# Performance work log

Measured on AMD Instinct MI355X. Metric: run time of the kernel, lower is better.

Reference implementation:

```python
import jax, jax.numpy as jnp
import numpy as np

VOCAB = 50257
EMBED = 128
N_HOPS = 3
MAX_STORY_LEN = 50


def setup_inputs() -> dict:
    key = jax.random.key(0)
    ks = jax.random.split(key, 10)
    B, n, T_c, T_q = 64, 50, 20, 20
    stories = jax.random.randint(ks[0], (B, n, T_c), 0, VOCAB)
    questions = jax.random.randint(ks[1], (B, T_q), 0, VOCAB)
    stories_masks = jax.random.randint(ks[2], (B, n, T_c), 0, 2)
    # Embedding tables, N(0, 0.1), padding_idx=0 row zeroed (as in torch nn.Embedding padding_idx)
    def emb(k, rows):
        w = 0.1 * jax.random.normal(k, (rows, EMBED), dtype=jnp.float32)
        return w.at[0].set(0.0)
    W_A = emb(ks[3], VOCAB)
    W_B = emb(ks[4], VOCAB)
    W_C = emb(ks[5], VOCAB)
    W_AT = emb(ks[6], MAX_STORY_LEN + 1)
    W_CT = emb(ks[7], MAX_STORY_LEN + 1)
    # nn.Linear(embed, vocab): weight [vocab, embed], bias [vocab]
    lim = 1.0 / np.sqrt(EMBED)
    W_lin = jax.random.uniform(ks[8], (VOCAB, EMBED), minval=-lim, maxval=lim, dtype=jnp.float32)
    b_lin = jax.random.uniform(ks[9], (VOCAB,), minval=-lim, maxval=lim, dtype=jnp.float32)
    return {"stories": stories, "questions": questions, "stories_masks": stories_masks,
            "W_A": W_A, "W_B": W_B, "W_C": W_C, "W_AT": W_AT, "W_CT": W_CT,
            "W_lin": W_lin, "b_lin": b_lin}


def reference(stories, questions, stories_masks, W_A, W_B, W_C, W_AT, W_CT, W_lin, b_lin):
    B, n, T_c = stories.shape
    # temporal index: sentence i -> i+1 if it contains any real token (mask==0), else 0 (padding)
    word_len = (stories_masks == 0).sum(axis=2)                      # [B, n]
    te_idx = jnp.arange(1, n + 1)[None, :] * (word_len >= 1)         # [B, n]
    # question embedding (basic encoding: sum over tokens)
    u = W_B[questions].sum(axis=1)                                   # [B, d]
    # memories/contexts: embeddings are identical every hop, compute once
    m = W_A[stories].sum(axis=2) + W_AT[te_idx]                      # [B, n, d]
    c = W_C[stories].sum(axis=2) + W_CT[te_idx]                      # [B, n, d]
    for _ in range(N_HOPS):
        score = jnp.einsum('bnd,bd->bn', m, u)                       # [B, n]
        probs = jax.nn.softmax(score, axis=1)
        o = jnp.einsum('bnd,bn->bd', c, probs)                       # [B, d]
        u = u + o
    return u @ W_lin.T + b_lin                                       # [B, vocab]
```

## Files before the change

kernel.cpp:

```cpp
#include <hip/hip_runtime.h>
#include <hip/hip_bf16.h>

#define VOCAB 50257
#define EMBED 128
#define NSENT 50
#define TC 20
#define TQ 20
#define BATCH 64
#define NHOPS 3

typedef __bf16 bf16x8 __attribute__((ext_vector_type(8)));
typedef float  f32x4v __attribute__((ext_vector_type(4)));

__global__ void __launch_bounds__(256) k_embed(
    const int* __restrict__ stories, const int* __restrict__ masks,
    const int* __restrict__ questions,
    const float* __restrict__ W_A, const float* __restrict__ W_B,
    const float* __restrict__ W_C,
    const float* __restrict__ W_AT, const float* __restrict__ W_CT,
    float* __restrict__ ws_m, float* __restrict__ ws_c, float* __restrict__ ws_u)
{
    const int blk = blockIdx.x;
    const int tid = threadIdx.x;
    if (blk < BATCH * NSENT) {
        const int b = blk / NSENT;
        const int i = blk % NSENT;
        const int* mrow = masks + (b * NSENT + i) * TC;
        int cnt = 0;
        #pragma unroll
        for (int t = 0; t < TC; t++) cnt += (mrow[t] == 0);
        const int te = (cnt >= 1) ? (i + 1) : 0;

        const int* srow = stories + (b * NSENT + i) * TC;
        const int table = tid >> 7;
        const int d = tid & 127;
        const float* T  = table ? W_C  : W_A;
        const float* TT = table ? W_CT : W_AT;
        float acc = TT[te * EMBED + d];
        #pragma unroll
        for (int t = 0; t < TC; t++) {
            const int tok = srow[t];
            acc += T[tok * EMBED + d];
        }
        float* dst = table ? ws_c : ws_m;
        dst[(b * NSENT + i) * EMBED + d] = acc;
    } else {
        const int b = blk - BATCH * NSENT;
        if (tid < EMBED) {
            const int* qrow = questions + b * TQ;
            float acc = 0.f;
            #pragma unroll
            for (int t = 0; t < TQ; t++) acc += W_B[qrow[t] * EMBED + tid];
            ws_u[b * EMBED + tid] = acc;
        }
    }
}

__global__ void __launch_bounds__(256) k_hops(
    const float* __restrict__ ws_m, const float* __restrict__ ws_c,
    const float* __restrict__ ws_u, __bf16* __restrict__ ws_ubf)
{
    __shared__ float smc[2 * NSENT * EMBED];
    __shared__ float su[EMBED];
    __shared__ float sp[64];
    __shared__ float ssc[64];

    const int b = blockIdx.x;
    const int tid = threadIdx.x;

    const f32x4v* gm = (const f32x4v*)(ws_m + b * NSENT * EMBED);
    const f32x4v* gc = (const f32x4v*)(ws_c + b * NSENT * EMBED);
    f32x4v* s4 = (f32x4v*)smc;
    for (int idx = tid; idx < NSENT * EMBED / 4; idx += 256) {
        s4[idx] = gm[idx];
        s4[NSENT * EMBED / 4 + idx] = gc[idx];
    }
    if (tid < EMBED) su[tid] = ws_u[b * EMBED + tid];
    __syncthreads();

    const int wave = tid >> 6, lane = tid & 63;
    for (int hop = 0; hop < NHOPS; hop++) {
        for (int i = wave; i < NSENT; i += 4) {
            float s = smc[i * EMBED + lane] * su[lane]
                    + smc[i * EMBED + 64 + lane] * su[64 + lane];
            #pragma unroll
            for (int off = 32; off >= 1; off >>= 1) s += __shfl_xor(s, off);
            if (lane == 0) ssc[i] = s;
        }
        __syncthreads();
        if (tid < 64) {
            float v = (tid < NSENT) ? ssc[tid] : -1e30f;
            float mx = v;
            #pragma unroll
            for (int off = 32; off >= 1; off >>= 1) mx = fmaxf(mx, __shfl_xor(mx, off));
            float e = (tid < NSENT) ? expf(v - mx) : 0.f;
            float sum = e;
            #pragma unroll
            for (int off = 32; off >= 1; off >>= 1) sum += __shfl_xor(sum, off);
            sp[tid] = e / sum;
        }
        __syncthreads();
        if (tid < EMBED) {
            float o = 0.f;
            for (int i = 0; i < NSENT; i++)
                o += smc[NSENT * EMBED + i * EMBED + tid] * sp[i];
            su[tid] += o;
        }
        __syncthreads();
    }
    if (tid < EMBED) ws_ubf[b * EMBED + tid] = (__bf16)su[tid];
}

__global__ void __launch_bounds__(256) k_out(
    const __bf16* __restrict__ u_bf, const float* __restrict__ W_lin,
    const float* __restrict__ b_lin, float* __restrict__ out)
{
    const int tid  = threadIdx.x;
    const int wave = tid >> 6, lane = tid & 63;
    const int m    = lane & 15;
    const int quad = lane >> 4;
    const int v0   = blockIdx.x * 64 + wave * 16;
    const int v    = v0 + m;
    const int vc   = (v < VOCAB) ? v : (VOCAB - 1);

    f32x4v acc[4] = { {0.f,0.f,0.f,0.f}, {0.f,0.f,0.f,0.f},
                      {0.f,0.f,0.f,0.f}, {0.f,0.f,0.f,0.f} };

    const float* wrow = W_lin + (long)vc * EMBED;
    #pragma unroll
    for (int kc = 0; kc < 4; kc++) {
        const int k0 = kc * 32 + quad * 8;
        f32x4v w0 = *(const f32x4v*)(wrow + k0);
        f32x4v w1 = *(const f32x4v*)(wrow + k0 + 4);
        bf16x8 wb;
        wb[0] = (__bf16)w0[0]; wb[1] = (__bf16)w0[1];
        wb[2] = (__bf16)w0[2]; wb[3] = (__bf16)w0[3];
        wb[4] = (__bf16)w1[0]; wb[5] = (__bf16)w1[1];
        wb[6] = (__bf16)w1[2]; wb[7] = (__bf16)w1[3];
        #pragma unroll
        for (int bt = 0; bt < 4; bt++) {
            bf16x8 ab = *(const bf16x8*)(u_bf + (bt * 16 + m) * EMBED + k0);
            acc[bt] = __builtin_amdgcn_mfma_f32_16x16x32_bf16(ab, wb, acc[bt], 0, 0, 0);
        }
    }

    const float bl = b_lin[vc];
    if (v < VOCAB) {
        #pragma unroll
        for (int bt = 0; bt < 4; bt++) {
            #pragma unroll
            for (int r = 0; r < 4; r++) {
                const int bb = bt * 16 + quad * 4 + r;
                out[(long)bb * VOCAB + v] = acc[bt][r] + bl;
            }
        }
    }
}

extern "C" void kernel_launch(void* const* d_in, const int* in_sizes, int n_in,
                              void* d_out, int out_size, void* d_ws, size_t ws_size,
                              hipStream_t stream) {
    const int*   stories   = (const int*)d_in[0];
    const int*   questions = (const int*)d_in[1];
    const int*   masks     = (const int*)d_in[2];
    const float* W_A       = (const float*)d_in[3];
    const float* W_B       = (const float*)d_in[4];
    const float* W_C       = (const float*)d_in[5];
    const float* W_AT      = (const float*)d_in[6];
    const float* W_CT      = (const float*)d_in[7];
    const float* W_lin     = (const float*)d_in[8];
    const float* b_lin     = (const float*)d_in[9];
    float* out = (float*)d_out;

    float* ws    = (float*)d_ws;
    float* ws_m  = ws;
    float* ws_c  = ws + BATCH * NSENT * EMBED;
    float* ws_u  = ws + 2 * BATCH * NSENT * EMBED;
    __bf16* ws_ubf = (__bf16*)(ws + 2 * BATCH * NSENT * EMBED + BATCH * EMBED);

    k_embed<<<dim3(BATCH * NSENT + BATCH), dim3(256), 0, stream>>>(
        stories, masks, questions, W_A, W_B, W_C, W_AT, W_CT, ws_m, ws_c, ws_u);
    k_hops<<<dim3(BATCH), dim3(256), 0, stream>>>(ws_m, ws_c, ws_u, ws_ubf);
    k_out<<<dim3((VOCAB + 63) / 64), dim3(256), 0, stream>>>(ws_ubf, W_lin, b_lin, out);
}
```

Measured before the change: 163.2 us.

## Vectorize embedding gathers, split hop reduction, stage output tile through LDS

The embedding kernel now gathers rows with float4 loads, with groups of 32 threads each summing a subset of tokens, and reduces the partial sums through shared memory. In the hop kernel all 256 threads take part in the weighted context sum, split across two halves of the sentences. The output GEMM handles 128 vocab columns per block, stages results in a padded shared tile, and writes coalesced rows with nontemporal stores. These target uncoalesced scalar gathers, idle threads, and the strided scattered output writes, at the cost of extra shared memory and block syncs.

Measured after the change: 161.7 us. No clear change (-0.9%).

```diff
diff --git a/kernel.cpp b/kernel.cpp
--- a/kernel.cpp
+++ b/kernel.cpp
@@ -20,8 +20,12 @@
     const float* __restrict__ W_AT, const float* __restrict__ W_CT,
     float* __restrict__ ws_m, float* __restrict__ ws_c, float* __restrict__ ws_u)
 {
+    __shared__ float sred[8][128];
     const int blk = blockIdx.x;
     const int tid = threadIdx.x;
+    const int grp = tid >> 5;
+    const int gl  = tid & 31;
+
     if (blk < BATCH * NSENT) {
         const int b = blk / NSENT;
         const int i = blk % NSENT;
@@ -32,26 +36,40 @@
         const int te = (cnt >= 1) ? (i + 1) : 0;
 
         const int* srow = stories + (b * NSENT + i) * TC;
-        const int table = tid >> 7;
-        const int d = tid & 127;
-        const float* T  = table ? W_C  : W_A;
-        const float* TT = table ? W_CT : W_AT;
-        float acc = TT[te * EMBED + d];
-        #pragma unroll
-        for (int t = 0; t < TC; t++) {
-            const int tok = srow[t];
-            acc += T[tok * EMBED + d];
-        }
-        float* dst = table ? ws_c : ws_m;
-        dst[(b * NSENT + i) * EMBED + d] = acc;
+        const int table = grp >> 2;
+        const int sub   = grp & 3;
+        const float* T = table ? W_C : W_A;
+
+        f32x4v acc = {0.f, 0.f, 0.f, 0.f};
+        #pragma unroll
+        for (int t = 0; t < 5; t++) {
+            const int tok = srow[sub + t * 4];
+            acc += *(const f32x4v*)(T + (long)tok * EMBED + gl * 4);
+        }
+        *(f32x4v*)&sred[grp][gl * 4] = acc;
+        __syncthreads();
+
+        const int tb = tid >> 7, d = tid & 127;
+        const float* TT = tb ? W_CT : W_AT;
+        float v = sred[tb * 4 + 0][d] + sred[tb * 4 + 1][d]
+                + sred[tb * 4 + 2][d] + sred[tb * 4 + 3][d]
+                + TT[te * EMBED + d];
+        float* dst = tb ? ws_c : ws_m;
+        dst[(b * NSENT + i) * EMBED + d] = v;
     } else {
         const int b = blk - BATCH * NSENT;
+        f32x4v acc = {0.f, 0.f, 0.f, 0.f};
+        for (int t = grp; t < TQ; t += 8) {
+            const int tok = questions[b * TQ + t];
+            acc += *(const f32x4v*)(W_B + (long)tok * EMBED + gl * 4);
+        }
+        *(f32x4v*)&sred[grp][gl * 4] = acc;
+        __syncthreads();
         if (tid < EMBED) {
-            const int* qrow = questions + b * TQ;
-            float acc = 0.f;
-            #pragma unroll
-            for (int t = 0; t < TQ; t++) acc += W_B[qrow[t] * EMBED + tid];
-            ws_u[b * EMBED + tid] = acc;
+            float v = 0.f;
+            #pragma unroll
+            for (int g = 0; g < 8; g++) v += sred[g][tid];
+            ws_u[b * EMBED + tid] = v;
         }
     }
 }
@@ -64,6 +82,7 @@
     __shared__ float su[EMBED];
     __shared__ float sp[64];
     __shared__ float ssc[64];
+    __shared__ float spo[2][EMBED];
 
     const int b = blockIdx.x;
     const int tid = threadIdx.x;
@@ -79,6 +98,7 @@
     __syncthreads();
 
     const int wave = tid >> 6, lane = tid & 63;
+    const int d128 = tid & 127, hf = tid >> 7;
     for (int hop = 0; hop < NHOPS; hop++) {
         for (int i = wave; i < NSENT; i += 4) {
             float s = smc[i * EMBED + lane] * su[lane]
@@ -100,59 +120,79 @@
             sp[tid] = e / sum;
         }
         __syncthreads();
-        if (tid < EMBED) {
+        {
             float o = 0.f;
-            for (int i = 0; i < NSENT; i++)
-                o += smc[NSENT * EMBED + i * EMBED + tid] * sp[i];
-            su[tid] += o;
-        }
+            #pragma unroll
+            for (int k = 0; k < 25; k++) {
+                const int i = hf * 25 + k;
+                o += smc[NSENT * EMBED + i * EMBED + d128] * sp[i];
+            }
+            spo[hf][d128] = o;
+        }
+        __syncthreads();
+        if (tid < EMBED) su[tid] += spo[0][tid] + spo[1][tid];
         __syncthreads();
     }
     if (tid < EMBED) ws_ubf[b * EMBED + tid] = (__bf16)su[tid];
 }
 
+#define VT 128
 __global__ void __launch_bounds__(256) k_out(
     const __bf16* __restrict__ u_bf, const float* __restrict__ W_lin,
     const float* __restrict__ b_lin, float* __restrict__ out)
 {
+    __shared__ float sT[64][VT + 1];
+
     const int tid  = threadIdx.x;
     const int wave = tid >> 6, lane = tid & 63;
     const int m    = lane & 15;
     const int quad = lane >> 4;
-    const int v0   = blockIdx.x * 64 + wave * 16;
-    const int v    = v0 + m;
-    const int vc   = (v < VOCAB) ? v : (VOCAB - 1);
-
-    f32x4v acc[4] = { {0.f,0.f,0.f,0.f}, {0.f,0.f,0.f,0.f},
-                      {0.f,0.f,0.f,0.f}, {0.f,0.f,0.f,0.f} };
-
-    const float* wrow = W_lin + (long)vc * EMBED;
+    const int vbase = blockIdx.x * VT + wave * 32;
+
+    f32x4v acc[2][4] = {};
+
     #pragma unroll
     for (int kc = 0; kc < 4; kc++) {
         const int k0 = kc * 32 + quad * 8;
-        f32x4v w0 = *(const f32x4v*)(wrow + k0);
-        f32x4v w1 = *(const f32x4v*)(wrow + k0 + 4);
-        bf16x8 wb;
-        wb[0] = (__bf16)w0[0]; wb[1] = (__bf16)w0[1];
-        wb[2] = (__bf16)w0[2]; wb[3] = (__bf16)w0[3];
-        wb[4] = (__bf16)w1[0]; wb[5] = (__bf16)w1[1];
-        wb[6] = (__bf16)w1[2]; wb[7] = (__bf16)w1[3];
+        bf16x8 wb[2];
+        #pragma unroll
+        for (int s = 0; s < 2; s++) {
+            int v = vbase + s * 16 + m;
+            int vc = (v < VOCAB) ? v : (VOCAB - 1);
+            const float* wrow = W_lin + (long)vc * EMBED;
+            f32x4v w0 = *(const f32x4v*)(wrow + k0);
+            f32x4v w1 = *(const f32x4v*)(wrow + k0 + 4);
+            wb[s][0] = (__bf16)w0[0]; wb[s][1] = (__bf16)w0[1];
+            wb[s][2] = (__bf16)w0[2]; wb[s][3] = (__bf16)w0[3];
+            wb[s][4] = (__bf16)w1[0]; wb[s][5] = (__bf16)w1[1];
+            wb[s][6] = (__bf16)w1[2]; wb[s][7] = (__bf16)w1[3];
+        }
         #pragma unroll
         for (int bt = 0; bt < 4; bt++) {
             bf16x8 ab = *(const bf16x8*)(u_bf + (bt * 16 + m) * EMBED + k0);
-            acc[bt] = __builtin_amdgcn_mfma_f32_16x16x32_bf16(ab, wb, acc[bt], 0, 0, 0);
-        }
-    }
-
-    const float bl = b_lin[vc];
+            acc[0][bt] = __builtin_amdgcn_mfma_f32_16x16x32_bf16(ab, wb[0], acc[0][bt], 0, 0, 0);
+            acc[1][bt] = __builtin_amdgcn_mfma_f32_16x16x32_bf16(ab, wb[1], acc[1][bt], 0, 0, 0);
+        }
+    }
+
+    #pragma unroll
+    for (int s = 0; s < 2; s++)
+        #pragma unroll
+        for (int bt = 0; bt < 4; bt++)
+            #pragma unroll
+            for (int r = 0; r < 4; r++)
+                sT[bt * 16 + quad * 4 + r][wave * 32 + s * 16 + m] = acc[s][bt][r];
+    __syncthreads();
+
+    const int col = tid & 127;
+    const int bh  = tid >> 7;
+    const int v   = blockIdx.x * VT + col;
     if (v < VOCAB) {
-        #pragma unroll
-        for (int bt = 0; bt < 4; bt++) {
-            #pragma unroll
-            for (int r = 0; r < 4; r++) {
-                const int bb = bt * 16 + quad * 4 + r;
-                out[(long)bb * VOCAB + v] = acc[bt][r] + bl;
-            }
+        const float bl = b_lin[v];
+        #pragma unroll
+        for (int it = 0; it < 32; it++) {
+            const int bb = bh * 32 + it;
+            __builtin_nontemporal_store(sT[bb][col] + bl, &out[(long)bb * VOCAB + v]);
         }
     }
 }
@@ -181,5 +221,5 @@
     k_embed<<<dim3(BATCH * NSENT + BATCH), dim3(256), 0, stream>>>(
         stories, masks, questions, W_A, W_B, W_C, W_AT, W_CT, ws_m, ws_c, ws_u);
     k_hops<<<dim3(BATCH), dim3(256), 0, stream>>>(ws_m, ws_c, ws_u, ws_ubf);
-    k_out<<<dim3((VOCAB + 63) / 64), dim3(256), 0, stream>>>(ws_ubf, W_lin, b_lin, out);
-}
+    k_out<<<dim3((VOCAB + VT - 1) / VT), dim3(256), 0, stream>>>(ws_ubf, W_lin, b_lin, out);
+}
```
